# Kernel optimization log

Hardware: AMD Instinct MI355X
Metric: run time of the kernel (lower is better)

The kernel has to match this reference:

```python
import jax, jax.numpy as jnp
import numpy as np

B, G, S, NNZ = 64, 20000, 200000, 2000000

def setup_inputs() -> dict:
    key = jax.random.key(0)
    k1, k2, k3, k4, k5 = jax.random.split(key, 5)
    x = jax.random.normal(k1, (B, G), dtype=jnp.float32)
    # COO connectivity: row = SNP index (output), col = gene index (input)
    row = jax.random.randint(k2, (NNZ,), 0, S, dtype=jnp.int64)
    col = jax.random.randint(k3, (NNZ,), 0, G, dtype=jnp.int64)
    index = jnp.stack([row, col])  # [2, NNZ]
    W_sparse = jax.random.normal(k4, (NNZ,), dtype=jnp.float32) * 0.02
    b = jax.random.normal(k5, (S, 1), dtype=jnp.float32) * 0.02
    return {"x": x, "W_sparse": W_sparse, "b": b, "index": index, "n_SNPs": S}

def reference(x, W_sparse, b, index, n_SNPs):
    # spmm: sparse [n_SNPs, n_genes] @ x.T [n_genes, B] -> [n_SNPs, B]
    row, col = index[0], index[1]
    gathered = x.T[col] * W_sparse[:, None]            # [NNZ, B] edge contributions
    dot_prod = jax.ops.segment_sum(gathered, row, num_segments=n_SNPs)  # [S, B]
    output = dot_prod + b                              # bias broadcast over batch
    return output.T                                    # [B, n_SNPs]
```

## Files before the change

### kernel.cpp

```cpp
#include <hip/hip_runtime.h>


#define WAVE 64
#define CHUNK 2048
#define RBITS 6
#define BINROWS 64
#define NBIN_PAD 3584
#define CAP_BIN 896
#define PREP_SMEM (CHUNK * 8 + NBIN_PAD * 4 + 16)

#define RL(v, i)  __builtin_amdgcn_readlane((int)(v), (i))
#define RLF(v, i) __int_as_float(__builtin_amdgcn_readlane(__float_as_int(v), (i)))

__device__ __forceinline__ int swz(int r, int b) {
    return (r << 6) + (b ^ (r & 63));
}

__device__ __forceinline__ unsigned short f2bf(float f) {
    unsigned u = __float_as_uint(f);
    unsigned r = (u + 0x7fffu + ((u >> 16) & 1u)) >> 16;
    return (unsigned short)r;
}

__global__ __launch_bounds__(256) void prep_kernel(
        const float* __restrict__ x, unsigned short* __restrict__ xTh,
        int G, int tgrid,
        const int* __restrict__ row, const int* __restrict__ col,
        const float* __restrict__ w, uint2* __restrict__ sedge1,
        unsigned* __restrict__ segtab, int nnz, int nbin) {
    __shared__ __align__(16) char smem[PREP_SMEM];
    const int t = threadIdx.x;

    if ((int)blockIdx.x < tgrid) {
        float (*tile)[65] = (float (*)[65])smem;
        const int g0 = blockIdx.x * 64;
        {
            const int j  = t & 63;
            const int b0 = t >> 6;
            if (g0 + j < G) {
                #pragma unroll
                for (int it = 0; it < 16; ++it) {
                    const int b = b0 + it * 4;
                    tile[j][b] = x[(size_t)b * G + g0 + j];
                }
            }
        }
        __syncthreads();
        {
            const int b  = t & 63;
            const int j0 = t >> 6;
            #pragma unroll
            for (int it = 0; it < 16; ++it) {
                const int j = j0 + it * 4;
                if (g0 + j < G) xTh[(size_t)(g0 + j) * WAVE + b] = f2bf(tile[j][b]);
            }
        }
        return;
    }

    uint2* stage = (uint2*)smem;
    int*   hist  = (int*)(smem + CHUNK * 8);
    int*   wpart = (int*)(smem + CHUNK * 8 + NBIN_PAD * 4);
    const int lane = t & 63;
    const int wv   = t >> 6;
    const int blk  = (int)blockIdx.x - tgrid;
    const int e0   = blk * CHUNK;
    const bool full = (e0 + CHUNK <= nnz);
    const int M    = full ? CHUNK : (nnz - e0);

    for (int j = t; j < NBIN_PAD; j += 256) hist[j] = 0;
    __syncthreads();

    int4 ra, rb, ca, cb; float4 wa, wb;
    if (full) {
        const int4*   rv = (const int4*)(row + e0);
        const int4*   cv = (const int4*)(col + e0);
        const float4* wf = (const float4*)(w + e0);
        ra = rv[t]; rb = rv[t + 256];
        ca = cv[t]; cb = cv[t + 256];
        wa = wf[t]; wb = wf[t + 256];
        atomicAdd(&hist[ra.x >> RBITS], 1);
        atomicAdd(&hist[ra.y >> RBITS], 1);
        atomicAdd(&hist[ra.z >> RBITS], 1);
        atomicAdd(&hist[ra.w >> RBITS], 1);
        atomicAdd(&hist[rb.x >> RBITS], 1);
        atomicAdd(&hist[rb.y >> RBITS], 1);
        atomicAdd(&hist[rb.z >> RBITS], 1);
        atomicAdd(&hist[rb.w >> RBITS], 1);
    } else {
        for (int k = 0; k < CHUNK / 256; ++k) {
            const int i = k * 256 + t;
            if (i < M) atomicAdd(&hist[row[e0 + i] >> RBITS], 1);
        }
    }
    __syncthreads();

    {
        int c[14];
        int p = 0;
        #pragma unroll
        for (int j = 0; j < 14; ++j) { c[j] = hist[t * 14 + j]; p += c[j]; }
        int incl = p;
        #pragma unroll
        for (int d = 1; d < 64; d <<= 1) {
            const int u = __shfl_up(incl, d);
            if (lane >= d) incl += u;
        }
        if (lane == 63) wpart[wv] = incl;
        __syncthreads();
        int base = incl - p;
        #pragma unroll
        for (int ww = 0; ww < 4; ++ww)
            if (ww < wv) base += wpart[ww];
        unsigned* st = segtab + (size_t)blk * (size_t)(nbin + 1);
        int run = base;
        #pragma unroll
        for (int j = 0; j < 14; ++j) {
            const int bj = t * 14 + j;
            hist[bj] = run;
            if (bj <= nbin) st[bj] = (unsigned)(e0 + run);
            run += c[j];
        }
    }
    __syncthreads();

#define PUT(r_, c_, w_)                                                       \
    {                                                                         \
        const int pos = atomicAdd(&hist[(r_) >> RBITS], 1);                   \
        stage[pos] = make_uint2(((unsigned)((r_) & 63) << 15) |               \
                                (unsigned)(c_), __float_as_uint(w_));         \
    }
    if (full) {
        PUT(ra.x, ca.x, wa.x) PUT(ra.y, ca.y, wa.y)
        PUT(ra.z, ca.z, wa.z) PUT(ra.w, ca.w, wa.w)
        PUT(rb.x, cb.x, wb.x) PUT(rb.y, cb.y, wb.y)
        PUT(rb.z, cb.z, wb.z) PUT(rb.w, cb.w, wb.w)
    } else {
        for (int k = 0; k < CHUNK / 256; ++k) {
            const int i = k * 256 + t;
            if (i < M) {
                const int r = row[e0 + i];
                PUT(r, col[e0 + i], w[e0 + i])
            }
        }
    }
#undef PUT
    __syncthreads();

    if (full) {
        const uint4* sg4 = (const uint4*)stage;
        uint4* o4 = (uint4*)(sedge1 + e0);
        #pragma unroll
        for (int k = 0; k < CHUNK / 512; ++k) o4[k * 256 + t] = sg4[k * 256 + t];
    } else {
        for (int j = t; j < M; j += 256) sedge1[e0 + j] = stage[j];
    }
}

#define PROC(Er, ar, ii)                                                      \
    {                                                                         \
        const int   k_ = RL((Er).x, (ii));                                    \
        const float w_ = __int_as_float(RL((Er).y, (ii)));                    \
        const float v_ = __uint_as_float(                                     \
            (unsigned)*(const unsigned short*)(xb + k_ + lane2) << 16);       \
        (ar) += v_ * w_;                                                      \
    }

__global__ __launch_bounds__(256) void compute_kernel(
        const unsigned short* __restrict__ xTh,
        const uint2* __restrict__ sedge1,
        const unsigned* __restrict__ segtab,
        const float* __restrict__ bias,
        float* __restrict__ out, int S, int nchunk, int nbin) {
    __shared__ float tile[64 * 64];
    __shared__ uint2 eds2[CAP_BIN];
    __shared__ int   rcnt[4][BINROWS];
    __shared__ int   cur[4][BINROWS];
    __shared__ int   rstart[BINROWS], rend[BINROWS];
    __shared__ int   spart[4];
    uint2* eds1 = (uint2*)tile;

    const int t    = threadIdx.x;
    const int lane = t & 63;
    const int wv   = t >> 6;

    const int nwg = nbin;
    const int q8 = nwg >> 3, r8 = nwg & 7;
    const int xcd = (int)blockIdx.x & 7, off = (int)blockIdx.x >> 3;
    const int b = (xcd < r8 ? xcd * (q8 + 1) : r8 * (q8 + 1) + (xcd - r8) * q8)
                  + off;
    const int r0 = b << RBITS;

    if (t < BINROWS) {
        rcnt[0][t] = 0; rcnt[1][t] = 0; rcnt[2][t] = 0; rcnt[3][t] = 0;
    }

    int st0 = 0, n0_ = 0, st1 = 0, n1_ = 0, st2 = 0, n2_ = 0, st3 = 0, n3_ = 0;
    {
        const size_t stride = (size_t)(nbin + 1);
        if (t < nchunk) {
            const unsigned* p = segtab + (size_t)t * stride + b;
            st0 = (int)p[0]; n0_ = (int)(p[1] - p[0]);
        }
        if (t + 256 < nchunk) {
            const unsigned* p = segtab + (size_t)(t + 256) * stride + b;
            st1 = (int)p[0]; n1_ = (int)(p[1] - p[0]);
        }
        if (t + 512 < nchunk) {
            const unsigned* p = segtab + (size_t)(t + 512) * stride + b;
            st2 = (int)p[0]; n2_ = (int)(p[1] - p[0]);
        }
        if (t + 768 < nchunk) {
            const unsigned* p = segtab + (size_t)(t + 768) * stride + b;
            st3 = (int)p[0]; n3_ = (int)(p[1] - p[0]);
        }
    }
    const int nt = n0_ + n1_ + n2_ + n3_;
    int incl = nt;
    #pragma unroll
    for (int d = 1; d < 64; d <<= 1) {
        const int u = __shfl_up(incl, d);
        if (lane >= d) incl += u;
    }
    if (lane == 63) spart[wv] = incl;
    __syncthreads();
    int base = incl - nt;
    #pragma unroll
    for (int ww = 0; ww < 4; ++ww)
        if (ww < wv) base += spart[ww];
    int M = spart[0] + spart[1] + spart[2] + spart[3];
    if (M > CAP_BIN) M = CAP_BIN;

    {
        int p = base;
        for (int k = 0; k < n0_; ++k, ++p)
            if (p < CAP_BIN) eds1[p] = sedge1[st0 + k];
        for (int k = 0; k < n1_; ++k, ++p)
            if (p < CAP_BIN) eds1[p] = sedge1[st1 + k];
        for (int k = 0; k < n2_; ++k, ++p)
            if (p < CAP_BIN) eds1[p] = sedge1[st2 + k];
        for (int k = 0; k < n3_; ++k, ++p)
            if (p < CAP_BIN) eds1[p] = sedge1[st3 + k];
    }
    __syncthreads();

    for (int i = t; i < M; i += 256)
        atomicAdd(&rcnt[wv][eds1[i].x >> 15], 1);
    __syncthreads();

    if (t < BINROWS) {
        const int c0 = rcnt[0][t], c1 = rcnt[1][t];
        const int c2 = rcnt[2][t], c3 = rcnt[3][t];
        const int tot = c0 + c1 + c2 + c3;
        int inc2 = tot;
        #pragma unroll
        for (int d = 1; d < 64; d <<= 1) {
            const int u = __shfl_up(inc2, d);
            if (lane >= d) inc2 += u;
        }
        const int stt = inc2 - tot;
        rstart[t] = stt;
        rend[t]   = stt + tot;
        cur[0][t] = stt;
        cur[1][t] = stt + c0;
        cur[2][t] = stt + c0 + c1;
        cur[3][t] = stt + c0 + c1 + c2;
    }
    __syncthreads();

    for (int i = t; i < M; i += 256) {
        const uint2 e = eds1[i];
        const int r = (int)(e.x >> 15);
        const int pos = atomicAdd(&cur[wv][r], 1);
        eds2[pos] = make_uint2((e.x & 0x7fffu) << 7, e.y);
    }
    __syncthreads();

    const char* xb = (const char*)xTh;
    const int lane2 = lane * 2;
    const int rw = r0 + wv * 16;
    float bv = 0.f;
    if (lane < 16 && rw + lane < S) bv = bias[rw + lane];

    #pragma unroll
    for (int qd = 0; qd < 4; ++qd) {
        const int rl = wv * 16 + qd * 4;
        int s0 = rstart[rl + 0], e0g = rend[rl + 0];
        int s1 = rstart[rl + 1], e1g = rend[rl + 1];
        int s2 = rstart[rl + 2], e2g = rend[rl + 2];
        int s3 = rstart[rl + 3], e3g = rend[rl + 3];
        float a0 = 0.f, a1 = 0.f, a2 = 0.f, a3 = 0.f;
        while ((s0 < e0g) || (s1 < e1g) || (s2 < e2g) || (s3 < e3g)) {
            const int m0 = min(WAVE, e0g - s0);
            const int m1 = min(WAVE, e1g - s1);
            const int m2 = min(WAVE, e2g - s2);
            const int m3 = min(WAVE, e3g - s3);
            uint2 E0 = make_uint2(0u, 0u), E1 = make_uint2(0u, 0u);
            uint2 E2 = make_uint2(0u, 0u), E3 = make_uint2(0u, 0u);
            if (lane < m0) E0 = eds2[s0 + lane];
            if (lane < m1) E1 = eds2[s1 + lane];
            if (lane < m2) E2 = eds2[s2 + lane];
            if (lane < m3) E3 = eds2[s3 + lane];
            const int mm = max(max(m0, m1), max(m2, m3));
            int i = 0;
            for (; i + 2 <= mm; i += 2) {
                PROC(E0, a0, i) PROC(E1, a1, i) PROC(E2, a2, i) PROC(E3, a3, i)
                PROC(E0, a0, i + 1) PROC(E1, a1, i + 1)
                PROC(E2, a2, i + 1) PROC(E3, a3, i + 1)
            }
            if (i < mm) {
                PROC(E0, a0, i) PROC(E1, a1, i) PROC(E2, a2, i) PROC(E3, a3, i)
            }
            s0 += max(m0, 0); s1 += max(m1, 0);
            s2 += max(m2, 0); s3 += max(m3, 0);
        }
        tile[swz(rl + 0, lane)] = a0 + RLF(bv, qd * 4 + 0);
        tile[swz(rl + 1, lane)] = a1 + RLF(bv, qd * 4 + 1);
        tile[swz(rl + 2, lane)] = a2 + RLF(bv, qd * 4 + 2);
        tile[swz(rl + 3, lane)] = a3 + RLF(bv, qd * 4 + 3);
    }
    __syncthreads();

    const int srow = r0 + lane;
    #pragma unroll
    for (int k = 0; k < 16; ++k) {
        const int bb = wv * 16 + k;
        if (srow < S) out[(size_t)bb * S + srow] = tile[swz(lane, bb)];
    }
}

extern "C" void kernel_launch(void* const* d_in, const int* in_sizes, int n_in,
                              void* d_out, int out_size, void* d_ws, size_t ws_size,
                              hipStream_t stream) {
    const float* x    = (const float*)d_in[0];
    const float* W    = (const float*)d_in[1];
    const float* bias = (const float*)d_in[2];
    const int*   idx  = (const int*)d_in[3];

    const int NNZ = in_sizes[1];
    const int S   = in_sizes[2];
    const int B   = out_size / S;
    const int G   = in_sizes[0] / B;
    const int* rowi = idx;
    const int* coli = idx + NNZ;
    float* out = (float*)d_out;

    const int nbin   = (S + BINROWS - 1) >> RBITS;
    const int nchunk = (NNZ + CHUNK - 1) / CHUNK;
    const int tgrid  = (G + 63) / 64;

    char* ws = (char*)d_ws;
    size_t o = 0;
    auto alloc = [&](size_t bytes) {
        void* p = ws + o;
        o = (o + bytes + 255) & ~(size_t)255;
        return p;
    };
    unsigned short* xTh = (unsigned short*)alloc((size_t)G * B * sizeof(unsigned short));
    uint2*    sedge1 = (uint2*)   alloc((size_t)NNZ * sizeof(uint2));
    unsigned* segtab = (unsigned*)alloc((size_t)nchunk * (size_t)(nbin + 1) *
                                        sizeof(unsigned));
    (void)ws_size; (void)n_in;

    prep_kernel<<<tgrid + nchunk, 256, 0, stream>>>(
        x, xTh, G, tgrid, rowi, coli, W, sedge1, segtab, NNZ, nbin);

    compute_kernel<<<nbin, 256, 0, stream>>>(xTh, sedge1, segtab, bias,
                                             out, S, nchunk, nbin);
}
```

Measured before the change: 179.3 us.

## Fuse prep and compute into persistent kernel with software grid barrier

Merges the transpose/binning prep kernel and the per-bin compute kernel into one persistent kernel sized to the occupancy-limited resident block count, separated by an atomic-counter grid barrier. Segment tables shrink to 16-bit chunk-relative offsets to cut table traffic. This removes the second launch and the inter-kernel gap, but adds a memset and spin-wait barrier, and the persistent loop may reduce per-bin occupancy or lose load balance.

Measured after the change: 351.4 us. +96.0%, slower.

```diff
diff --git a/kernel.cpp b/kernel.cpp
--- a/kernel.cpp
+++ b/kernel.cpp
@@ -7,7 +7,7 @@
 #define BINROWS 64
 #define NBIN_PAD 3584
 #define CAP_BIN 896
-#define PREP_SMEM (CHUNK * 8 + NBIN_PAD * 4 + 16)
+#define SMEM_BYTES 30752
 
 #define RL(v, i)  __builtin_amdgcn_readlane((int)(v), (i))
 #define RLF(v, i) __int_as_float(__builtin_amdgcn_readlane(__float_as_int(v), (i)))
@@ -22,139 +22,16 @@
     return (unsigned short)r;
 }
 
-__global__ __launch_bounds__(256) void prep_kernel(
-        const float* __restrict__ x, unsigned short* __restrict__ xTh,
-        int G, int tgrid,
-        const int* __restrict__ row, const int* __restrict__ col,
-        const float* __restrict__ w, uint2* __restrict__ sedge1,
-        unsigned* __restrict__ segtab, int nnz, int nbin) {
-    __shared__ __align__(16) char smem[PREP_SMEM];
-    const int t = threadIdx.x;
-
-    if ((int)blockIdx.x < tgrid) {
-        float (*tile)[65] = (float (*)[65])smem;
-        const int g0 = blockIdx.x * 64;
-        {
-            const int j  = t & 63;
-            const int b0 = t >> 6;
-            if (g0 + j < G) {
-                #pragma unroll
-                for (int it = 0; it < 16; ++it) {
-                    const int b = b0 + it * 4;
-                    tile[j][b] = x[(size_t)b * G + g0 + j];
-                }
-            }
-        }
-        __syncthreads();
-        {
-            const int b  = t & 63;
-            const int j0 = t >> 6;
-            #pragma unroll
-            for (int it = 0; it < 16; ++it) {
-                const int j = j0 + it * 4;
-                if (g0 + j < G) xTh[(size_t)(g0 + j) * WAVE + b] = f2bf(tile[j][b]);
-            }
-        }
-        return;
-    }
-
-    uint2* stage = (uint2*)smem;
-    int*   hist  = (int*)(smem + CHUNK * 8);
-    int*   wpart = (int*)(smem + CHUNK * 8 + NBIN_PAD * 4);
-    const int lane = t & 63;
-    const int wv   = t >> 6;
-    const int blk  = (int)blockIdx.x - tgrid;
-    const int e0   = blk * CHUNK;
-    const bool full = (e0 + CHUNK <= nnz);
-    const int M    = full ? CHUNK : (nnz - e0);
-
-    for (int j = t; j < NBIN_PAD; j += 256) hist[j] = 0;
+__device__ __forceinline__ void grid_barrier(int* bar, int nb) {
     __syncthreads();
-
-    int4 ra, rb, ca, cb; float4 wa, wb;
-    if (full) {
-        const int4*   rv = (const int4*)(row + e0);
-        const int4*   cv = (const int4*)(col + e0);
-        const float4* wf = (const float4*)(w + e0);
-        ra = rv[t]; rb = rv[t + 256];
-        ca = cv[t]; cb = cv[t + 256];
-        wa = wf[t]; wb = wf[t + 256];
-        atomicAdd(&hist[ra.x >> RBITS], 1);
-        atomicAdd(&hist[ra.y >> RBITS], 1);
-        atomicAdd(&hist[ra.z >> RBITS], 1);
-        atomicAdd(&hist[ra.w >> RBITS], 1);
-        atomicAdd(&hist[rb.x >> RBITS], 1);
-        atomicAdd(&hist[rb.y >> RBITS], 1);
-        atomicAdd(&hist[rb.z >> RBITS], 1);
-        atomicAdd(&hist[rb.w >> RBITS], 1);
-    } else {
-        for (int k = 0; k < CHUNK / 256; ++k) {
-            const int i = k * 256 + t;
-            if (i < M) atomicAdd(&hist[row[e0 + i] >> RBITS], 1);
-        }
+    if (threadIdx.x == 0) {
+        __threadfence();
+        atomicAdd(bar, 1);
+        while (__hip_atomic_load(bar, __ATOMIC_ACQUIRE,
+                                 __HIP_MEMORY_SCOPE_AGENT) < nb)
+            __builtin_amdgcn_s_sleep(2);
     }
     __syncthreads();
-
-    {
-        int c[14];
-        int p = 0;
-        #pragma unroll
-        for (int j = 0; j < 14; ++j) { c[j] = hist[t * 14 + j]; p += c[j]; }
-        int incl = p;
-        #pragma unroll
-        for (int d = 1; d < 64; d <<= 1) {
-            const int u = __shfl_up(incl, d);
-            if (lane >= d) incl += u;
-        }
-        if (lane == 63) wpart[wv] = incl;
-        __syncthreads();
-        int base = incl - p;
-        #pragma unroll
-        for (int ww = 0; ww < 4; ++ww)
-            if (ww < wv) base += wpart[ww];
-        unsigned* st = segtab + (size_t)blk * (size_t)(nbin + 1);
-        int run = base;
-        #pragma unroll
-        for (int j = 0; j < 14; ++j) {
-            const int bj = t * 14 + j;
-            hist[bj] = run;
-            if (bj <= nbin) st[bj] = (unsigned)(e0 + run);
-            run += c[j];
-        }
-    }
-    __syncthreads();
-
-#define PUT(r_, c_, w_)                                                       \
-    {                                                                         \
-        const int pos = atomicAdd(&hist[(r_) >> RBITS], 1);                   \
-        stage[pos] = make_uint2(((unsigned)((r_) & 63) << 15) |               \
-                                (unsigned)(c_), __float_as_uint(w_));         \
-    }
-    if (full) {
-        PUT(ra.x, ca.x, wa.x) PUT(ra.y, ca.y, wa.y)
-        PUT(ra.z, ca.z, wa.z) PUT(ra.w, ca.w, wa.w)
-        PUT(rb.x, cb.x, wb.x) PUT(rb.y, cb.y, wb.y)
-        PUT(rb.z, cb.z, wb.z) PUT(rb.w, cb.w, wb.w)
-    } else {
-        for (int k = 0; k < CHUNK / 256; ++k) {
-            const int i = k * 256 + t;
-            if (i < M) {
-                const int r = row[e0 + i];
-                PUT(r, col[e0 + i], w[e0 + i])
-            }
-        }
-    }
-#undef PUT
-    __syncthreads();
-
-    if (full) {
-        const uint4* sg4 = (const uint4*)stage;
-        uint4* o4 = (uint4*)(sedge1 + e0);
-        #pragma unroll
-        for (int k = 0; k < CHUNK / 512; ++k) o4[k * 256 + t] = sg4[k * 256 + t];
-    } else {
-        for (int j = t; j < M; j += 256) sedge1[e0 + j] = stage[j];
-    }
 }
 
 #define PROC(Er, ar, ii)                                                      \
@@ -166,166 +43,307 @@
         (ar) += v_ * w_;                                                      \
     }
 
-__global__ __launch_bounds__(256) void compute_kernel(
-        const unsigned short* __restrict__ xTh,
-        const uint2* __restrict__ sedge1,
-        const unsigned* __restrict__ segtab,
-        const float* __restrict__ bias,
-        float* __restrict__ out, int S, int nchunk, int nbin) {
-    __shared__ float tile[64 * 64];
-    __shared__ uint2 eds2[CAP_BIN];
-    __shared__ int   rcnt[4][BINROWS];
-    __shared__ int   cur[4][BINROWS];
-    __shared__ int   rstart[BINROWS], rend[BINROWS];
-    __shared__ int   spart[4];
-    uint2* eds1 = (uint2*)tile;
-
+__global__ __launch_bounds__(256) void fused_kernel(
+        const float* __restrict__ x, unsigned short* __restrict__ xTh,
+        int G, int tgrid,
+        const int* __restrict__ row, const int* __restrict__ col,
+        const float* __restrict__ w,
+        uint2* __restrict__ sedge1, unsigned short* __restrict__ seg16,
+        const float* __restrict__ bias, float* __restrict__ out,
+        int S, int nnz, int nbin, int nchunk, int NB, int* __restrict__ bar) {
+    __shared__ __align__(16) char smem[SMEM_BYTES];
     const int t    = threadIdx.x;
     const int lane = t & 63;
     const int wv   = t >> 6;
 
-    const int nwg = nbin;
-    const int q8 = nwg >> 3, r8 = nwg & 7;
-    const int xcd = (int)blockIdx.x & 7, off = (int)blockIdx.x >> 3;
-    const int b = (xcd < r8 ? xcd * (q8 + 1) : r8 * (q8 + 1) + (xcd - r8) * q8)
-                  + off;
-    const int r0 = b << RBITS;
-
-    if (t < BINROWS) {
-        rcnt[0][t] = 0; rcnt[1][t] = 0; rcnt[2][t] = 0; rcnt[3][t] = 0;
-    }
-
-    int st0 = 0, n0_ = 0, st1 = 0, n1_ = 0, st2 = 0, n2_ = 0, st3 = 0, n3_ = 0;
-    {
-        const size_t stride = (size_t)(nbin + 1);
-        if (t < nchunk) {
-            const unsigned* p = segtab + (size_t)t * stride + b;
-            st0 = (int)p[0]; n0_ = (int)(p[1] - p[0]);
-        }
-        if (t + 256 < nchunk) {
-            const unsigned* p = segtab + (size_t)(t + 256) * stride + b;
-            st1 = (int)p[0]; n1_ = (int)(p[1] - p[0]);
-        }
-        if (t + 512 < nchunk) {
-            const unsigned* p = segtab + (size_t)(t + 512) * stride + b;
-            st2 = (int)p[0]; n2_ = (int)(p[1] - p[0]);
-        }
-        if (t + 768 < nchunk) {
-            const unsigned* p = segtab + (size_t)(t + 768) * stride + b;
-            st3 = (int)p[0]; n3_ = (int)(p[1] - p[0]);
-        }
-    }
-    const int nt = n0_ + n1_ + n2_ + n3_;
-    int incl = nt;
-    #pragma unroll
-    for (int d = 1; d < 64; d <<= 1) {
-        const int u = __shfl_up(incl, d);
-        if (lane >= d) incl += u;
-    }
-    if (lane == 63) spart[wv] = incl;
-    __syncthreads();
-    int base = incl - nt;
-    #pragma unroll
-    for (int ww = 0; ww < 4; ++ww)
-        if (ww < wv) base += spart[ww];
-    int M = spart[0] + spart[1] + spart[2] + spart[3];
-    if (M > CAP_BIN) M = CAP_BIN;
-
-    {
-        int p = base;
-        for (int k = 0; k < n0_; ++k, ++p)
-            if (p < CAP_BIN) eds1[p] = sedge1[st0 + k];
-        for (int k = 0; k < n1_; ++k, ++p)
-            if (p < CAP_BIN) eds1[p] = sedge1[st1 + k];
-        for (int k = 0; k < n2_; ++k, ++p)
-            if (p < CAP_BIN) eds1[p] = sedge1[st2 + k];
-        for (int k = 0; k < n3_; ++k, ++p)
-            if (p < CAP_BIN) eds1[p] = sedge1[st3 + k];
-    }
-    __syncthreads();
-
-    for (int i = t; i < M; i += 256)
-        atomicAdd(&rcnt[wv][eds1[i].x >> 15], 1);
-    __syncthreads();
-
-    if (t < BINROWS) {
-        const int c0 = rcnt[0][t], c1 = rcnt[1][t];
-        const int c2 = rcnt[2][t], c3 = rcnt[3][t];
-        const int tot = c0 + c1 + c2 + c3;
-        int inc2 = tot;
+    const int nwork1 = tgrid + nchunk;
+    for (int itw = blockIdx.x; itw < nwork1; itw += NB) {
+        __syncthreads();
+        if (itw < tgrid) {
+            float (*tile)[65] = (float (*)[65])smem;
+            const int g0 = itw * 64;
+            {
+                const int j  = t & 63;
+                const int b0 = t >> 6;
+                if (g0 + j < G) {
+                    #pragma unroll
+                    for (int it = 0; it < 16; ++it) {
+                        const int b = b0 + it * 4;
+                        tile[j][b] = x[(size_t)b * G + g0 + j];
+                    }
+                }
+            }
+            __syncthreads();
+            {
+                const int b  = t & 63;
+                const int j0 = t >> 6;
+                #pragma unroll
+                for (int it = 0; it < 16; ++it) {
+                    const int j = j0 + it * 4;
+                    if (g0 + j < G)
+                        xTh[(size_t)(g0 + j) * WAVE + b] = f2bf(tile[j][b]);
+                }
+            }
+        } else {
+            uint2* stage = (uint2*)smem;
+            int*   hist  = (int*)(smem + CHUNK * 8);
+            int*   wpart = (int*)(smem + CHUNK * 8 + NBIN_PAD * 4);
+            const int blk  = itw - tgrid;
+            const int e0   = blk * CHUNK;
+            const bool full = (e0 + CHUNK <= nnz);
+            const int M    = full ? CHUNK : (nnz - e0);
+
+            for (int j = t; j < NBIN_PAD; j += 256) hist[j] = 0;
+            __syncthreads();
+
+            int4 ra, rb, ca, cb; float4 wa, wb;
+            if (full) {
+                const int4*   rv = (const int4*)(row + e0);
+                const int4*   cv = (const int4*)(col + e0);
+                const float4* wf = (const float4*)(w + e0);
+                ra = rv[t]; rb = rv[t + 256];
+                ca = cv[t]; cb = cv[t + 256];
+                wa = wf[t]; wb = wf[t + 256];
+                atomicAdd(&hist[ra.x >> RBITS], 1);
+                atomicAdd(&hist[ra.y >> RBITS], 1);
+                atomicAdd(&hist[ra.z >> RBITS], 1);
+                atomicAdd(&hist[ra.w >> RBITS], 1);
+                atomicAdd(&hist[rb.x >> RBITS], 1);
+                atomicAdd(&hist[rb.y >> RBITS], 1);
+                atomicAdd(&hist[rb.z >> RBITS], 1);
+                atomicAdd(&hist[rb.w >> RBITS], 1);
+            } else {
+                for (int k = 0; k < CHUNK / 256; ++k) {
+                    const int i = k * 256 + t;
+                    if (i < M) atomicAdd(&hist[row[e0 + i] >> RBITS], 1);
+                }
+            }
+            __syncthreads();
+
+            {
+                int c[14];
+                int p = 0;
+                #pragma unroll
+                for (int j = 0; j < 14; ++j) { c[j] = hist[t * 14 + j]; p += c[j]; }
+                int incl = p;
+                #pragma unroll
+                for (int d = 1; d < 64; d <<= 1) {
+                    const int u = __shfl_up(incl, d);
+                    if (lane >= d) incl += u;
+                }
+                if (lane == 63) wpart[wv] = incl;
+                __syncthreads();
+                int base = incl - p;
+                #pragma unroll
+                for (int ww = 0; ww < 4; ++ww)
+                    if (ww < wv) base += wpart[ww];
+                unsigned short* st = seg16 + (size_t)blk * (size_t)(nbin + 1);
+                int run = base;
+                #pragma unroll
+                for (int j = 0; j < 14; ++j) {
+                    const int bj = t * 14 + j;
+                    hist[bj] = run;
+                    if (bj <= nbin) st[bj] = (unsigned short)run;
+                    run += c[j];
+                }
+            }
+            __syncthreads();
+
+#define PUT(r_, c_, w_)                                                       \
+    {                                                                         \
+        const int pos = atomicAdd(&hist[(r_) >> RBITS], 1);                   \
+        stage[pos] = make_uint2(((unsigned)((r_) & 63) << 15) |               \
+                                (unsigned)(c_), __float_as_uint(w_));         \
+    }
+            if (full) {
+                PUT(ra.x, ca.x, wa.x) PUT(ra.y, ca.y, wa.y)
+                PUT(ra.z, ca.z, wa.z) PUT(ra.w, ca.w, wa.w)
+                PUT(rb.x, cb.x, wb.x) PUT(rb.y, cb.y, wb.y)
+                PUT(rb.z, cb.z, wb.z) PUT(rb.w, cb.w, wb.w)
+            } else {
+                for (int k = 0; k < CHUNK / 256; ++k) {
+                    const int i = k * 256 + t;
+                    if (i < M) {
+                        const int r = row[e0 + i];
+                        PUT(r, col[e0 + i], w[e0 + i])
+                    }
+                }
+            }
+#undef PUT
+            __syncthreads();
+
+            if (full) {
+                const uint4* sg4 = (const uint4*)stage;
+                uint4* o4 = (uint4*)(sedge1 + e0);
+                #pragma unroll
+                for (int k = 0; k < CHUNK / 512; ++k)
+                    o4[k * 256 + t] = sg4[k * 256 + t];
+            } else {
+                for (int j = t; j < M; j += 256) sedge1[e0 + j] = stage[j];
+            }
+        }
+    }
+
+    grid_barrier(bar, NB);
+
+    float* tile  = (float*)smem;
+    uint2* eds2  = (uint2*)(smem + 16384);
+    int (*rcnt)[BINROWS] = (int (*)[BINROWS])(smem + 23552);
+    int (*cur)[BINROWS]  = (int (*)[BINROWS])(smem + 24576);
+    int* rstart = (int*)(smem + 25600);
+    int* rend   = (int*)(smem + 25856);
+    int* spart  = (int*)(smem + 26112);
+    uint2* eds1 = (uint2*)smem;
+
+    const char* xb = (const char*)xTh;
+    const int lane2 = lane * 2;
+    const size_t stride = (size_t)(nbin + 1);
+
+    for (int iw = blockIdx.x; iw < nbin; iw += NB) {
+        __syncthreads();
+
+        const int q8 = nbin >> 3, r8 = nbin & 7;
+        const int xcd = iw & 7, off = iw >> 3;
+        const int b = (xcd < r8 ? xcd * (q8 + 1)
+                                : r8 * (q8 + 1) + (xcd - r8) * q8) + off;
+        const int r0 = b << RBITS;
+
+        if (t < BINROWS) {
+            rcnt[0][t] = 0; rcnt[1][t] = 0; rcnt[2][t] = 0; rcnt[3][t] = 0;
+        }
+
+        int st0 = 0, n0_ = 0, st1 = 0, n1_ = 0;
+        int st2 = 0, n2_ = 0, st3 = 0, n3_ = 0;
+        {
+            if (t < nchunk) {
+                const unsigned short* p = seg16 + (size_t)t * stride + b;
+                st0 = t * CHUNK + (int)p[0]; n0_ = (int)p[1] - (int)p[0];
+            }
+            if (t + 256 < nchunk) {
+                const unsigned short* p = seg16 + (size_t)(t + 256) * stride + b;
+                st1 = (t + 256) * CHUNK + (int)p[0]; n1_ = (int)p[1] - (int)p[0];
+            }
+            if (t + 512 < nchunk) {
+                const unsigned short* p = seg16 + (size_t)(t + 512) * stride + b;
+                st2 = (t + 512) * CHUNK + (int)p[0]; n2_ = (int)p[1] - (int)p[0];
+            }
+            if (t + 768 < nchunk) {
+                const unsigned short* p = seg16 + (size_t)(t + 768) * stride + b;
+                st3 = (t + 768) * CHUNK + (int)p[0]; n3_ = (int)p[1] - (int)p[0];
+            }
+        }
+        const int nt = n0_ + n1_ + n2_ + n3_;
+        int incl = nt;
         #pragma unroll
         for (int d = 1; d < 64; d <<= 1) {
-            const int u = __shfl_up(inc2, d);
-            if (lane >= d) inc2 += u;
-        }
-        const int stt = inc2 - tot;
-        rstart[t] = stt;
-        rend[t]   = stt + tot;
-        cur[0][t] = stt;
-        cur[1][t] = stt + c0;
-        cur[2][t] = stt + c0 + c1;
-        cur[3][t] = stt + c0 + c1 + c2;
-    }
-    __syncthreads();
-
-    for (int i = t; i < M; i += 256) {
-        const uint2 e = eds1[i];
-        const int r = (int)(e.x >> 15);
-        const int pos = atomicAdd(&cur[wv][r], 1);
-        eds2[pos] = make_uint2((e.x & 0x7fffu) << 7, e.y);
-    }
-    __syncthreads();
-
-    const char* xb = (const char*)xTh;
-    const int lane2 = lane * 2;
-    const int rw = r0 + wv * 16;
-    float bv = 0.f;
-    if (lane < 16 && rw + lane < S) bv = bias[rw + lane];
-
-    #pragma unroll
-    for (int qd = 0; qd < 4; ++qd) {
-        const int rl = wv * 16 + qd * 4;
-        int s0 = rstart[rl + 0], e0g = rend[rl + 0];
-        int s1 = rstart[rl + 1], e1g = rend[rl + 1];
-        int s2 = rstart[rl + 2], e2g = rend[rl + 2];
-        int s3 = rstart[rl + 3], e3g = rend[rl + 3];
-        float a0 = 0.f, a1 = 0.f, a2 = 0.f, a3 = 0.f;
-        while ((s0 < e0g) || (s1 < e1g) || (s2 < e2g) || (s3 < e3g)) {
-            const int m0 = min(WAVE, e0g - s0);
-            const int m1 = min(WAVE, e1g - s1);
-            const int m2 = min(WAVE, e2g - s2);
-            const int m3 = min(WAVE, e3g - s3);
-            uint2 E0 = make_uint2(0u, 0u), E1 = make_uint2(0u, 0u);
-            uint2 E2 = make_uint2(0u, 0u), E3 = make_uint2(0u, 0u);
-            if (lane < m0) E0 = eds2[s0 + lane];
-            if (lane < m1) E1 = eds2[s1 + lane];
-            if (lane < m2) E2 = eds2[s2 + lane];
-            if (lane < m3) E3 = eds2[s3 + lane];
-            const int mm = max(max(m0, m1), max(m2, m3));
-            int i = 0;
-            for (; i + 2 <= mm; i += 2) {
-                PROC(E0, a0, i) PROC(E1, a1, i) PROC(E2, a2, i) PROC(E3, a3, i)
-                PROC(E0, a0, i + 1) PROC(E1, a1, i + 1)
-                PROC(E2, a2, i + 1) PROC(E3, a3, i + 1)
-            }
-            if (i < mm) {
-                PROC(E0, a0, i) PROC(E1, a1, i) PROC(E2, a2, i) PROC(E3, a3, i)
-            }
-            s0 += max(m0, 0); s1 += max(m1, 0);
-            s2 += max(m2, 0); s3 += max(m3, 0);
-        }
-        tile[swz(rl + 0, lane)] = a0 + RLF(bv, qd * 4 + 0);
-        tile[swz(rl + 1, lane)] = a1 + RLF(bv, qd * 4 + 1);
-        tile[swz(rl + 2, lane)] = a2 + RLF(bv, qd * 4 + 2);
-        tile[swz(rl + 3, lane)] = a3 + RLF(bv, qd * 4 + 3);
-    }
-    __syncthreads();
-
-    const int srow = r0 + lane;
-    #pragma unroll
-    for (int k = 0; k < 16; ++k) {
-        const int bb = wv * 16 + k;
-        if (srow < S) out[(size_t)bb * S + srow] = tile[swz(lane, bb)];
+            const int u = __shfl_up(incl, d);
+            if (lane >= d) incl += u;
+        }
+        if (lane == 63) spart[wv] = incl;
+        __syncthreads();
+        int base = incl - nt;
+        #pragma unroll
+        for (int ww = 0; ww < 4; ++ww)
+            if (ww < wv) base += spart[ww];
+        int M = spart[0] + spart[1] + spart[2] + spart[3];
+        if (M > CAP_BIN) M = CAP_BIN;
+
+        {
+            int p = base;
+            for (int k = 0; k < n0_; ++k, ++p)
+                if (p < CAP_BIN) eds1[p] = sedge1[st0 + k];
+            for (int k = 0; k < n1_; ++k, ++p)
+                if (p < CAP_BIN) eds1[p] = sedge1[st1 + k];
+            for (int k = 0; k < n2_; ++k, ++p)
+                if (p < CAP_BIN) eds1[p] = sedge1[st2 + k];
+            for (int k = 0; k < n3_; ++k, ++p)
+                if (p < CAP_BIN) eds1[p] = sedge1[st3 + k];
+        }
+        __syncthreads();
+
+        for (int i = t; i < M; i += 256)
+            atomicAdd(&rcnt[wv][eds1[i].x >> 15], 1);
+        __syncthreads();
+
+        if (t < BINROWS) {
+            const int c0 = rcnt[0][t], c1 = rcnt[1][t];
+            const int c2 = rcnt[2][t], c3 = rcnt[3][t];
+            const int tot = c0 + c1 + c2 + c3;
+            int inc2 = tot;
+            #pragma unroll
+            for (int d = 1; d < 64; d <<= 1) {
+                const int u = __shfl_up(inc2, d);
+                if (lane >= d) inc2 += u;
+            }
+            const int stt = inc2 - tot;
+            rstart[t] = stt;
+            rend[t]   = stt + tot;
+            cur[0][t] = stt;
+            cur[1][t] = stt + c0;
+            cur[2][t] = stt + c0 + c1;
+            cur[3][t] = stt + c0 + c1 + c2;
+        }
+        __syncthreads();
+
+        for (int i = t; i < M; i += 256) {
+            const uint2 e = eds1[i];
+            const int r = (int)(e.x >> 15);
+            const int pos = atomicAdd(&cur[wv][r], 1);
+            eds2[pos] = make_uint2((e.x & 0x7fffu) << 7, e.y);
+        }
+        __syncthreads();
+
+        const int rw = r0 + wv * 16;
+        float bv = 0.f;
+        if (lane < 16 && rw + lane < S) bv = bias[rw + lane];
+
+        #pragma unroll
+        for (int qd = 0; qd < 4; ++qd) {
+            const int rl = wv * 16 + qd * 4;
+            int s0 = rstart[rl + 0], e0g = rend[rl + 0];
+            int s1 = rstart[rl + 1], e1g = rend[rl + 1];
+            int s2 = rstart[rl + 2], e2g = rend[rl + 2];
+            int s3 = rstart[rl + 3], e3g = rend[rl + 3];
+            float a0 = 0.f, a1 = 0.f, a2 = 0.f, a3 = 0.f;
+            while ((s0 < e0g) || (s1 < e1g) || (s2 < e2g) || (s3 < e3g)) {
+                const int m0 = min(WAVE, e0g - s0);
+                const int m1 = min(WAVE, e1g - s1);
+                const int m2 = min(WAVE, e2g - s2);
+                const int m3 = min(WAVE, e3g - s3);
+                uint2 E0 = make_uint2(0u, 0u), E1 = make_uint2(0u, 0u);
+                uint2 E2 = make_uint2(0u, 0u), E3 = make_uint2(0u, 0u);
+                if (lane < m0) E0 = eds2[s0 + lane];
+                if (lane < m1) E1 = eds2[s1 + lane];
+                if (lane < m2) E2 = eds2[s2 + lane];
+                if (lane < m3) E3 = eds2[s3 + lane];
+                const int mm = max(max(m0, m1), max(m2, m3));
+                int i = 0;
+                for (; i + 2 <= mm; i += 2) {
+                    PROC(E0, a0, i) PROC(E1, a1, i)
+                    PROC(E2, a2, i) PROC(E3, a3, i)
+                    PROC(E0, a0, i + 1) PROC(E1, a1, i + 1)
+                    PROC(E2, a2, i + 1) PROC(E3, a3, i + 1)
+                }
+                if (i < mm) {
+                    PROC(E0, a0, i) PROC(E1, a1, i)
+                    PROC(E2, a2, i) PROC(E3, a3, i)
+                }
+                s0 += max(m0, 0); s1 += max(m1, 0);
+                s2 += max(m2, 0); s3 += max(m3, 0);
+            }
+            tile[swz(rl + 0, lane)] = a0 + RLF(bv, qd * 4 + 0);
+            tile[swz(rl + 1, lane)] = a1 + RLF(bv, qd * 4 + 1);
+            tile[swz(rl + 2, lane)] = a2 + RLF(bv, qd * 4 + 2);
+            tile[swz(rl + 3, lane)] = a3 + RLF(bv, qd * 4 + 3);
+        }
+        __syncthreads();
+
+        const int srow = r0 + lane;
+        #pragma unroll
+        for (int k = 0; k < 16; ++k) {
+            const int bb = wv * 16 + k;
+            if (srow < S) out[(size_t)bb * S + srow] = tile[swz(lane, bb)];
+        }
     }
 }
 
@@ -356,15 +374,32 @@
         o = (o + bytes + 255) & ~(size_t)255;
         return p;
     };
+    int* bar = (int*)alloc(256);
     unsigned short* xTh = (unsigned short*)alloc((size_t)G * B * sizeof(unsigned short));
-    uint2*    sedge1 = (uint2*)   alloc((size_t)NNZ * sizeof(uint2));
-    unsigned* segtab = (unsigned*)alloc((size_t)nchunk * (size_t)(nbin + 1) *
-                                        sizeof(unsigned));
+    uint2* sedge1 = (uint2*)alloc((size_t)NNZ * sizeof(uint2));
+    unsigned short* seg16 = (unsigned short*)alloc(
+        (size_t)nchunk * (size_t)(nbin + 1) * sizeof(unsigned short));
     (void)ws_size; (void)n_in;
 
-    prep_kernel<<<tgrid + nchunk, 256, 0, stream>>>(
-        x, xTh, G, tgrid, rowi, coli, W, sedge1, segtab, NNZ, nbin);
-
-    compute_kernel<<<nbin, 256, 0, stream>>>(xTh, sedge1, segtab, bias,
-                                             out, S, nchunk, nbin);
+    static int NB = -1;
+    if (NB < 0) {
+        int dev = 0;
+        (void)hipGetDevice(&dev);
+        int ncu = 0;
+        if (hipDeviceGetAttribute(&ncu, hipDeviceAttributeMultiprocessorCount,
+                                  dev) != hipSuccess || ncu <= 0)
+            ncu = 256;
+        int bpc = 0;
+        if (hipOccupancyMaxActiveBlocksPerMultiprocessor(&bpc, fused_kernel,
+                                                         256, 0) != hipSuccess ||
+            bpc < 1)
+            bpc = 1;
+        NB = ncu * bpc;
+        if (NB > 8192) NB = 8192;
+    }
+
+    hipMemsetAsync(bar, 0, sizeof(int), stream);
+    fused_kernel<<<NB, 256, 0, stream>>>(
+        x, xTh, G, tgrid, rowi, coli, W, sedge1, seg16, bias, out,
+        S, NNZ, nbin, nchunk, NB, bar);
 }
```
